# Performance work log

Hardware: AMD Instinct MI355X
Metric: run time of the kernel (lower is better)

The kernel has to match this reference:

```python
import jax, jax.numpy as jnp
import numpy as np

LORA_ALPHA = 2.0

def setup_inputs() -> dict:
    key = jax.random.key(0)
    k1, k2, k3, k4 = jax.random.split(key, 4)
    B, S, D_IN, D_OUT, R = 4, 2048, 4096, 4096, 16
    x = jax.random.normal(k1, (B, S, D_IN), dtype=jnp.float32)
    weight = jax.random.normal(k2, (D_OUT, D_IN), dtype=jnp.float32) * (1.0 / np.sqrt(D_IN))
    lora_A = jax.random.normal(k3, (R, D_IN), dtype=jnp.float32) * (1.0 / np.sqrt(D_IN))
    lora_B = jax.random.normal(k4, (D_OUT, R), dtype=jnp.float32) * 0.02
    return {"x": x, "weight": weight, "lora_A": lora_A, "lora_B": lora_B}

def reference(x, weight, lora_A, lora_B):
    # main_out = F.linear(x, weight) = x @ weight.T
    main_out = jnp.einsum('bsd,od->bso', x, weight)
    # Faithful to source: materialize lora_weight = B @ A (out x in), then full linear
    lora_weight = lora_B @ lora_A  # [out, in]
    lora_out = jnp.einsum('bsd,od->bso', x, lora_weight) * LORA_ALPHA
    return main_out + lora_out
```

## Files before the change

### kernel.cpp

```cpp
#include <hip/hip_runtime.h>
#include <stdint.h>

typedef __attribute__((ext_vector_type(8))) short bf16x8;
typedef __attribute__((ext_vector_type(4))) float f32x4;

#define GM 8192
#define GN 4096
#define GK 4096
#define KT32 (GK / 32)

__device__ __forceinline__ unsigned short f2bf(float f) {
  union { float f; unsigned int u; } c; c.f = f;
  unsigned int u = c.u;
  unsigned int r = u + 0x7FFFu + ((u >> 16) & 1u);
  return (unsigned short)(r >> 16);
}

__global__ __launch_bounds__(256) void cvt_x_kernel(const float* __restrict__ x,
                                                    unsigned short* __restrict__ xb) {
  int i = blockIdx.x * 256 + threadIdx.x;
  const float4* p = (const float4*)x + (size_t)i * 2;
  float4 a = p[0], b = p[1];
  unsigned short t[8] = { f2bf(a.x), f2bf(a.y), f2bf(a.z), f2bf(a.w),
                          f2bf(b.x), f2bf(b.y), f2bf(b.z), f2bf(b.w) };
  int4 pk; __builtin_memcpy(&pk, t, 16);
  ((int4*)xb)[i] = pk;
}

__global__ __launch_bounds__(256) void weff_kernel(const float* __restrict__ w,
                                                   const float* __restrict__ lA,
                                                   const float* __restrict__ lB,
                                                   unsigned short* __restrict__ wb) {
  const int K = GK;
  int idx = blockIdx.x * 256 + threadIdx.x;
  int cg = idx & 511;
  int rg = idx >> 9;
  int i0 = cg << 3;
  int o0 = rg << 3;

  float acc[8][8];
#pragma unroll
  for (int r = 0; r < 8; ++r)
#pragma unroll
    for (int c = 0; c < 8; ++c) acc[r][c] = 0.f;

#pragma unroll
  for (int r = 0; r < 16; ++r) {
    float4 a0 = *(const float4*)(lA + (size_t)r * K + i0);
    float4 a1 = *(const float4*)(lA + (size_t)r * K + i0 + 4);
    float av[8] = { a0.x, a0.y, a0.z, a0.w, a1.x, a1.y, a1.z, a1.w };
#pragma unroll
    for (int row = 0; row < 8; ++row) {
      float b = lB[(size_t)(o0 + row) * 16 + r];
#pragma unroll
      for (int c = 0; c < 8; ++c) acc[row][c] += b * av[c];
    }
  }

#pragma unroll
  for (int row = 0; row < 8; ++row) {
    float4 w0 = *(const float4*)(w + (size_t)(o0 + row) * K + i0);
    float4 w1 = *(const float4*)(w + (size_t)(o0 + row) * K + i0 + 4);
    unsigned short t[8] = {
      f2bf(w0.x + 2.0f * acc[row][0]), f2bf(w0.y + 2.0f * acc[row][1]),
      f2bf(w0.z + 2.0f * acc[row][2]), f2bf(w0.w + 2.0f * acc[row][3]),
      f2bf(w1.x + 2.0f * acc[row][4]), f2bf(w1.y + 2.0f * acc[row][5]),
      f2bf(w1.z + 2.0f * acc[row][6]), f2bf(w1.w + 2.0f * acc[row][7]) };
    int4 pk; __builtin_memcpy(&pk, t, 16);
    *(int4*)(wb + (size_t)(o0 + row) * K + i0) = pk;
  }
}


__device__ __forceinline__ void gload16(const unsigned short* g, char* l) {
  __builtin_amdgcn_global_load_lds((__attribute__((address_space(1))) void*)g,
                                   (__attribute__((address_space(3))) void*)l, 16, 0, 0);
}

__device__ __forceinline__ void bar() {
  asm volatile("" ::: "memory");
  __builtin_amdgcn_s_barrier();
  asm volatile("" ::: "memory");
}

template <int N>
__device__ __forceinline__ void vmwait() {
  if constexpr (N == 0)      asm volatile("s_waitcnt vmcnt(0)" ::: "memory");
  else if constexpr (N == 4) asm volatile("s_waitcnt vmcnt(4)" ::: "memory");
}

#define MFMA_BF16(a, b, c) __builtin_amdgcn_mfma_f32_16x16x32_bf16((a), (b), (c), 0, 0, 0)

template <int BUF>
__device__ __forceinline__ void stage_tile(const unsigned short* A, const unsigned short* B,
                                           char* smem, int bm0, int bn0, int w, int lane,
                                           int kt) {
  const int gcol = ((lane & 3) * 8) ^ ((lane & 32) ? 16 : 0);
  const int r = lane >> 2;
#pragma unroll
  for (int i = 0; i < 2; ++i) {
    const int sr = 2 * w + i;
    gload16(A + (size_t)(bm0 + sr * 16 + r) * GK + kt * 32 + gcol,
            smem + BUF * 32768 + (sr << 10));
    gload16(B + (size_t)(bn0 + sr * 16 + r) * GK + kt * 32 + gcol,
            smem + BUF * 32768 + 16384 + (sr << 10));
  }
}

__device__ __forceinline__ bf16x8 ldsA(const char* smem, int buf, int sr, int foff) {
  return *(const bf16x8*)(smem + buf * 32768 + (sr << 10) + foff);
}
__device__ __forceinline__ bf16x8 ldsB(const char* smem, int buf, int sr, int foff) {
  return *(const bf16x8*)(smem + buf * 32768 + 16384 + (sr << 10) + foff);
}

template <int BUF, int TAIL>
__device__ __forceinline__ void phase(const unsigned short* __restrict__ A,
                                      const unsigned short* __restrict__ B,
                                      char* smem, int bm0, int bn0, int w, int lane,
                                      int wm, int wn, int foff, int kt,
                                      f32x4 (&acc)[8][4]) {
  if constexpr (TAIL == 0)
    stage_tile<(BUF + 2) & 3>(A, B, smem, bm0, bn0, w, lane, kt + 2);

  bf16x8 av[8], bv[4];
#pragma unroll
  for (int mi = 0; mi < 8; ++mi) av[mi] = ldsA(smem, BUF, wm * 8 + mi, foff);
#pragma unroll
  for (int ni = 0; ni < 4; ++ni) bv[ni] = ldsB(smem, BUF, wn * 4 + ni, foff);

  if constexpr (TAIL == 0)      vmwait<4>();
  else if constexpr (TAIL == 1) vmwait<0>();
  bar();

  __builtin_amdgcn_s_setprio(1);
#pragma unroll
  for (int mi = 0; mi < 8; ++mi)
#pragma unroll
    for (int ni = 0; ni < 4; ++ni)
      acc[mi][ni] = MFMA_BF16(av[mi], bv[ni], acc[mi][ni]);
  __builtin_amdgcn_s_setprio(0);
}

__global__ __launch_bounds__(512, 2) void gemm_bt_kernel(const unsigned short* __restrict__ A,
                                                         const unsigned short* __restrict__ B,
                                                         float* __restrict__ C) {
  __shared__ alignas(16) char smem[131072];

  const int t = threadIdx.x, lane = t & 63, w = t >> 6;
  const int wm = w >> 2, wn = w & 3;

  const int bid = blockIdx.x;
  const int wg  = (bid & 7) * (512 / 8) + (bid >> 3);
  const int bx = wg & 15, by = wg >> 4;
  const int bm0 = by * 256, bn0 = bx * 256;

  int foff = (lane & 15) * 64 + ((lane >> 4) << 4);
  foff ^= ((foff >> 9) & 1) << 5;

  stage_tile<0>(A, B, smem, bm0, bn0, w, lane, 0);
  stage_tile<1>(A, B, smem, bm0, bn0, w, lane, 1);
  vmwait<4>();
  bar();

  f32x4 acc[8][4] = {};

  for (int kt = 0; kt < KT32 - 4; kt += 4) {
    phase<0, 0>(A, B, smem, bm0, bn0, w, lane, wm, wn, foff, kt,     acc);
    phase<1, 0>(A, B, smem, bm0, bn0, w, lane, wm, wn, foff, kt + 1, acc);
    phase<2, 0>(A, B, smem, bm0, bn0, w, lane, wm, wn, foff, kt + 2, acc);
    phase<3, 0>(A, B, smem, bm0, bn0, w, lane, wm, wn, foff, kt + 3, acc);
  }
  phase<0, 0>(A, B, smem, bm0, bn0, w, lane, wm, wn, foff, KT32 - 4, acc);
  phase<1, 0>(A, B, smem, bm0, bn0, w, lane, wm, wn, foff, KT32 - 3, acc);
  phase<2, 1>(A, B, smem, bm0, bn0, w, lane, wm, wn, foff, KT32 - 2, acc);
  phase<3, 2>(A, B, smem, bm0, bn0, w, lane, wm, wn, foff, KT32 - 1, acc);

  const int orow = (lane >> 4) << 2;
#pragma unroll
  for (int mi = 0; mi < 8; ++mi) {
#pragma unroll
    for (int ni = 0; ni < 4; ++ni) {
      float* cp = C + (size_t)(bm0 + wm * 128 + mi * 16 + orow) * GN
                    + (bn0 + wn * 64 + ni * 16 + (lane & 15));
#pragma unroll
      for (int r = 0; r < 4; ++r)
        cp[(size_t)r * GN] = acc[mi][ni][r];
    }
  }
}

extern "C" void kernel_launch(void* const* d_in, const int* in_sizes, int n_in,
                              void* d_out, int out_size, void* d_ws, size_t ws_size,
                              hipStream_t stream) {
  const float* x  = (const float*)d_in[0];
  const float* w  = (const float*)d_in[1];
  const float* lA = (const float*)d_in[2];
  const float* lB = (const float*)d_in[3];
  float* out = (float*)d_out;

  const int M = GM, N = GN, K = GK;

  unsigned short* xb = (unsigned short*)d_ws;
  unsigned short* wb = xb + (size_t)M * K;

  cvt_x_kernel<<<dim3((M * K / 8) / 256), dim3(256), 0, stream>>>(x, xb);
  weff_kernel<<<dim3((N / 8) * (K / 8) / 256), dim3(256), 0, stream>>>(w, lA, lB, wb);
  gemm_bt_kernel<<<dim3((M / 256) * (N / 256)), dim3(512), 0, stream>>>(xb, wb, out);
}
```

Before: 293.6 us.

## Shrink GEMM block tile to 256x128 with triple-buffered LDS pipeline

Halves the block's N tile to 128 and the per-wave tile to 64x64. It switches from four to three LDS stage buffers, cutting shared memory from 128KB to 72KB so more blocks can be resident per CU. Loop unrolling and wait counts are adjusted for the 3-stage ring, and an explicit lgkmcnt wait is added before the barrier. This trades lower per-block data reuse (more global/L2 traffic per FLOP) for higher occupancy and latency hiding.

Result: slower. 340.3 us (+15.9%).

```diff
diff --git a/kernel.cpp b/kernel.cpp
--- a/kernel.cpp
+++ b/kernel.cpp
@@ -86,7 +86,11 @@
 template <int N>
 __device__ __forceinline__ void vmwait() {
   if constexpr (N == 0)      asm volatile("s_waitcnt vmcnt(0)" ::: "memory");
-  else if constexpr (N == 4) asm volatile("s_waitcnt vmcnt(4)" ::: "memory");
+  else if constexpr (N == 3) asm volatile("s_waitcnt vmcnt(3)" ::: "memory");
+}
+
+__device__ __forceinline__ void lgkm0() {
+  asm volatile("s_waitcnt lgkmcnt(0)" ::: "memory");
 }
 
 #define MFMA_BF16(a, b, c) __builtin_amdgcn_mfma_f32_16x16x32_bf16((a), (b), (c), 0, 0, 0)
@@ -97,91 +101,87 @@
                                            int kt) {
   const int gcol = ((lane & 3) * 8) ^ ((lane & 32) ? 16 : 0);
   const int r = lane >> 2;
-#pragma unroll
-  for (int i = 0; i < 2; ++i) {
-    const int sr = 2 * w + i;
-    gload16(A + (size_t)(bm0 + sr * 16 + r) * GK + kt * 32 + gcol,
-            smem + BUF * 32768 + (sr << 10));
-    gload16(B + (size_t)(bn0 + sr * 16 + r) * GK + kt * 32 + gcol,
-            smem + BUF * 32768 + 16384 + (sr << 10));
-  }
+  char* base = smem + BUF * 24576;
+  gload16(A + (size_t)(bm0 + (2 * w) * 16 + r) * GK + kt * 32 + gcol, base + ((2 * w) << 10));
+  gload16(A + (size_t)(bm0 + (2 * w + 1) * 16 + r) * GK + kt * 32 + gcol, base + ((2 * w + 1) << 10));
+  gload16(B + (size_t)(bn0 + w * 16 + r) * GK + kt * 32 + gcol, base + 16384 + (w << 10));
 }
 
 __device__ __forceinline__ bf16x8 ldsA(const char* smem, int buf, int sr, int foff) {
-  return *(const bf16x8*)(smem + buf * 32768 + (sr << 10) + foff);
+  return *(const bf16x8*)(smem + buf * 24576 + (sr << 10) + foff);
 }
 __device__ __forceinline__ bf16x8 ldsB(const char* smem, int buf, int sr, int foff) {
-  return *(const bf16x8*)(smem + buf * 32768 + 16384 + (sr << 10) + foff);
-}
-
-template <int BUF, int TAIL>
+  return *(const bf16x8*)(smem + buf * 24576 + 16384 + (sr << 10) + foff);
+}
+
+template <int BUF>
 __device__ __forceinline__ void phase(const unsigned short* __restrict__ A,
                                       const unsigned short* __restrict__ B,
                                       char* smem, int bm0, int bn0, int w, int lane,
                                       int wm, int wn, int foff, int kt,
-                                      f32x4 (&acc)[8][4]) {
-  if constexpr (TAIL == 0)
-    stage_tile<(BUF + 2) & 3>(A, B, smem, bm0, bn0, w, lane, kt + 2);
-
-  bf16x8 av[8], bv[4];
-#pragma unroll
-  for (int mi = 0; mi < 8; ++mi) av[mi] = ldsA(smem, BUF, wm * 8 + mi, foff);
+                                      f32x4 (&acc)[4][4]) {
+  if (kt + 2 < KT32)
+    stage_tile<(BUF + 2) % 3>(A, B, smem, bm0, bn0, w, lane, kt + 2);
+
+  bf16x8 av[4], bv[4];
+#pragma unroll
+  for (int mi = 0; mi < 4; ++mi) av[mi] = ldsA(smem, BUF, wm * 4 + mi, foff);
 #pragma unroll
   for (int ni = 0; ni < 4; ++ni) bv[ni] = ldsB(smem, BUF, wn * 4 + ni, foff);
 
-  if constexpr (TAIL == 0)      vmwait<4>();
-  else if constexpr (TAIL == 1) vmwait<0>();
+  if (kt + 2 < KT32)      vmwait<3>();
+  else if (kt + 1 < KT32) vmwait<0>();
+  lgkm0();
   bar();
 
   __builtin_amdgcn_s_setprio(1);
 #pragma unroll
-  for (int mi = 0; mi < 8; ++mi)
+  for (int mi = 0; mi < 4; ++mi)
 #pragma unroll
     for (int ni = 0; ni < 4; ++ni)
       acc[mi][ni] = MFMA_BF16(av[mi], bv[ni], acc[mi][ni]);
   __builtin_amdgcn_s_setprio(0);
 }
 
-__global__ __launch_bounds__(512, 2) void gemm_bt_kernel(const unsigned short* __restrict__ A,
+__global__ __launch_bounds__(512, 4) void gemm_bt_kernel(const unsigned short* __restrict__ A,
                                                          const unsigned short* __restrict__ B,
                                                          float* __restrict__ C) {
-  __shared__ alignas(16) char smem[131072];
+  __shared__ alignas(16) char smem[73728];
 
   const int t = threadIdx.x, lane = t & 63, w = t >> 6;
-  const int wm = w >> 2, wn = w & 3;
+  const int wm = w >> 1, wn = w & 1;
 
   const int bid = blockIdx.x;
-  const int wg  = (bid & 7) * (512 / 8) + (bid >> 3);
-  const int bx = wg & 15, by = wg >> 4;
-  const int bm0 = by * 256, bn0 = bx * 256;
+  const int wg  = (bid & 7) * (1024 / 8) + (bid >> 3);
+  const int bx = wg & 31, by = wg >> 5;
+  const int bm0 = by * 256, bn0 = bx * 128;
 
   int foff = (lane & 15) * 64 + ((lane >> 4) << 4);
   foff ^= ((foff >> 9) & 1) << 5;
 
   stage_tile<0>(A, B, smem, bm0, bn0, w, lane, 0);
   stage_tile<1>(A, B, smem, bm0, bn0, w, lane, 1);
-  vmwait<4>();
+  vmwait<3>();
   bar();
 
-  f32x4 acc[8][4] = {};
-
-  for (int kt = 0; kt < KT32 - 4; kt += 4) {
-    phase<0, 0>(A, B, smem, bm0, bn0, w, lane, wm, wn, foff, kt,     acc);
-    phase<1, 0>(A, B, smem, bm0, bn0, w, lane, wm, wn, foff, kt + 1, acc);
-    phase<2, 0>(A, B, smem, bm0, bn0, w, lane, wm, wn, foff, kt + 2, acc);
-    phase<3, 0>(A, B, smem, bm0, bn0, w, lane, wm, wn, foff, kt + 3, acc);
-  }
-  phase<0, 0>(A, B, smem, bm0, bn0, w, lane, wm, wn, foff, KT32 - 4, acc);
-  phase<1, 0>(A, B, smem, bm0, bn0, w, lane, wm, wn, foff, KT32 - 3, acc);
-  phase<2, 1>(A, B, smem, bm0, bn0, w, lane, wm, wn, foff, KT32 - 2, acc);
-  phase<3, 2>(A, B, smem, bm0, bn0, w, lane, wm, wn, foff, KT32 - 1, acc);
+  f32x4 acc[4][4] = {};
+
+  int kt = 0;
+  while (kt + 3 <= KT32) {
+    phase<0>(A, B, smem, bm0, bn0, w, lane, wm, wn, foff, kt,     acc);
+    phase<1>(A, B, smem, bm0, bn0, w, lane, wm, wn, foff, kt + 1, acc);
+    phase<2>(A, B, smem, bm0, bn0, w, lane, wm, wn, foff, kt + 2, acc);
+    kt += 3;
+  }
+  phase<0>(A, B, smem, bm0, bn0, w, lane, wm, wn, foff, 126, acc);
+  phase<1>(A, B, smem, bm0, bn0, w, lane, wm, wn, foff, 127, acc);
 
   const int orow = (lane >> 4) << 2;
 #pragma unroll
-  for (int mi = 0; mi < 8; ++mi) {
+  for (int mi = 0; mi < 4; ++mi) {
 #pragma unroll
     for (int ni = 0; ni < 4; ++ni) {
-      float* cp = C + (size_t)(bm0 + wm * 128 + mi * 16 + orow) * GN
+      float* cp = C + (size_t)(bm0 + wm * 64 + mi * 16 + orow) * GN
                     + (bn0 + wn * 64 + ni * 16 + (lane & 15));
 #pragma unroll
       for (int r = 0; r < 4; ++r)
@@ -206,5 +206,5 @@
 
   cvt_x_kernel<<<dim3((M * K / 8) / 256), dim3(256), 0, stream>>>(x, xb);
   weff_kernel<<<dim3((N / 8) * (K / 8) / 256), dim3(256), 0, stream>>>(w, lA, lB, wb);
-  gemm_bt_kernel<<<dim3((M / 256) * (N / 256)), dim3(512), 0, stream>>>(xb, wb, out);
-}
+  gemm_bt_kernel<<<dim3((M / 256) * (N / 128)), dim3(512), 0, stream>>>(xb, wb, out);
+}
```

## Switch GEMM to 32x32x16 MFMA with 64-wide K tiles and split staging

Applied to the files above, without the earlier changes.

Replaces the 16x16x32 bf16 MFMA tiling with 32x32x16 MFMA fragments, halving fragment loads per flop. K tiles grow to 64 with double-buffered 64KB stages, and each tile is staged in four interleaved quarter-loads spread across the compute phases. The aim is higher MFMA throughput per LDS read and smoother overlap of global-to-LDS loads with compute. The cost is more complex synchronisation, with one barrier per phase, and a changed epilogue write pattern.

New measurement: 321.6 us. +9.5%, slower.

```diff
diff --git a/kernel.cpp b/kernel.cpp
--- a/kernel.cpp
+++ b/kernel.cpp
@@ -2,12 +2,12 @@
 #include <stdint.h>
 
 typedef __attribute__((ext_vector_type(8))) short bf16x8;
-typedef __attribute__((ext_vector_type(4))) float f32x4;
+typedef __attribute__((ext_vector_type(16))) float f32x16;
 
 #define GM 8192
 #define GN 4096
 #define GK 4096
-#define KT32 (GK / 32)
+#define KTILES (GK / 64)
 
 __device__ __forceinline__ unsigned short f2bf(float f) {
   union { float f; unsigned int u; } c; c.f = f;
@@ -86,60 +86,92 @@
 template <int N>
 __device__ __forceinline__ void vmwait() {
   if constexpr (N == 0)      asm volatile("s_waitcnt vmcnt(0)" ::: "memory");
-  else if constexpr (N == 4) asm volatile("s_waitcnt vmcnt(4)" ::: "memory");
-}
-
-#define MFMA_BF16(a, b, c) __builtin_amdgcn_mfma_f32_16x16x32_bf16((a), (b), (c), 0, 0, 0)
-
-template <int BUF>
-__device__ __forceinline__ void stage_tile(const unsigned short* A, const unsigned short* B,
+  else if constexpr (N == 2) asm volatile("s_waitcnt vmcnt(2)" ::: "memory");
+}
+
+#define MFMA32(a, b, c) __builtin_amdgcn_mfma_f32_32x32x16_bf16((a), (b), (c), 0, 0, 0)
+
+template <int ISB, int SC, int BUF>
+__device__ __forceinline__ void stage_half(const unsigned short* A, const unsigned short* B,
                                            char* smem, int bm0, int bn0, int w, int lane,
                                            int kt) {
+  const unsigned short* mat = ISB ? B : A;
+  const int mbase = ISB ? bn0 : bm0;
   const int gcol = ((lane & 3) * 8) ^ ((lane & 32) ? 16 : 0);
-  const int r = lane >> 2;
 #pragma unroll
   for (int i = 0; i < 2; ++i) {
     const int sr = 2 * w + i;
-    gload16(A + (size_t)(bm0 + sr * 16 + r) * GK + kt * 32 + gcol,
-            smem + BUF * 32768 + (sr << 10));
-    gload16(B + (size_t)(bn0 + sr * 16 + r) * GK + kt * 32 + gcol,
-            smem + BUF * 32768 + 16384 + (sr << 10));
-  }
-}
-
-__device__ __forceinline__ bf16x8 ldsA(const char* smem, int buf, int sr, int foff) {
-  return *(const bf16x8*)(smem + buf * 32768 + (sr << 10) + foff);
-}
-__device__ __forceinline__ bf16x8 ldsB(const char* smem, int buf, int sr, int foff) {
-  return *(const bf16x8*)(smem + buf * 32768 + 16384 + (sr << 10) + foff);
-}
-
-template <int BUF, int TAIL>
-__device__ __forceinline__ void phase(const unsigned short* __restrict__ A,
+    const unsigned short* src = mat + (size_t)(mbase + sr * 16 + (lane >> 2)) * GK
+                                    + kt * 64 + SC * 32 + gcol;
+    char* dst = smem + BUF * 65536 + ISB * 32768 + ((sr * 2 + SC) << 10);
+    gload16(src, dst);
+  }
+}
+
+__device__ __forceinline__ bf16x8 ldsFrag(const char* smem, int byteOff) {
+  return *(const bf16x8*)(smem + byteOff);
+}
+
+template <int CUR, int TAIL>
+__device__ __forceinline__ void ktile(const unsigned short* __restrict__ A,
                                       const unsigned short* __restrict__ B,
                                       char* smem, int bm0, int bn0, int w, int lane,
-                                      int wm, int wn, int foff, int kt,
-                                      f32x4 (&acc)[8][4]) {
-  if constexpr (TAIL == 0)
-    stage_tile<(BUF + 2) & 3>(A, B, smem, bm0, bn0, w, lane, kt + 2);
-
-  bf16x8 av[8], bv[4];
-#pragma unroll
-  for (int mi = 0; mi < 8; ++mi) av[mi] = ldsA(smem, BUF, wm * 8 + mi, foff);
-#pragma unroll
-  for (int ni = 0; ni < 4; ++ni) bv[ni] = ldsB(smem, BUF, wn * 4 + ni, foff);
-
-  if constexpr (TAIL == 0)      vmwait<4>();
+                                      int wm, int wn, int kt,
+                                      f32x16 (&acc)[4][2]) {
+  constexpr int NXT = CUR ^ 1;
+  const int rlo = lane & 15, sub2 = (lane >> 4) & 1, khalf = lane >> 5;
+  const int m32 = (rlo & 8) << 2;
+
+  bf16x8 av[4], bv[2];
+
+#define READ_PHASE(PH, BUF)                                                            \
+  {                                                                                    \
+    constexpr int SC = (PH) >> 1;                                                      \
+    const int kin = ((PH) & 1) * 32 + khalf * 16;                                      \
+    const int roff = (rlo * 64 + kin) ^ m32;                                           \
+    _Pragma("unroll")                                                                  \
+    for (int mi = 0; mi < 4; ++mi)                                                     \
+      av[mi] = ldsFrag(smem, (BUF) * 65536 +                                           \
+                       (((wm * 8 + mi * 2 + sub2) * 2 + SC) << 10) + roff);            \
+    _Pragma("unroll")                                                                  \
+    for (int ni = 0; ni < 2; ++ni)                                                     \
+      bv[ni] = ldsFrag(smem, (BUF) * 65536 + 32768 +                                   \
+                       (((wn * 4 + ni * 2 + sub2) * 2 + SC) << 10) + roff);            \
+  }
+
+#define MFMA_PHASE()                                                                   \
+  __builtin_amdgcn_s_setprio(1);                                                       \
+  _Pragma("unroll")                                                                    \
+  for (int mi = 0; mi < 4; ++mi) {                                                     \
+    acc[mi][0] = MFMA32(av[mi], bv[0], acc[mi][0]);                                    \
+    acc[mi][1] = MFMA32(av[mi], bv[1], acc[mi][1]);                                    \
+  }                                                                                    \
+  __builtin_amdgcn_s_setprio(0);
+
+  if constexpr (TAIL < 2) stage_half<1, 0, NXT>(A, B, smem, bm0, bn0, w, lane, kt + 1);
+  READ_PHASE(0, CUR);
+  bar();
+  MFMA_PHASE();
+
+  if constexpr (TAIL < 2) stage_half<0, 1, NXT>(A, B, smem, bm0, bn0, w, lane, kt + 1);
+  READ_PHASE(1, CUR);
+  bar();
+  MFMA_PHASE();
+
+  if constexpr (TAIL < 2) stage_half<1, 1, NXT>(A, B, smem, bm0, bn0, w, lane, kt + 1);
+  READ_PHASE(2, CUR);
+  bar();
+  MFMA_PHASE();
+
+  if constexpr (TAIL == 0) stage_half<0, 0, CUR>(A, B, smem, bm0, bn0, w, lane, kt + 2);
+  READ_PHASE(3, CUR);
+  if constexpr (TAIL == 0)      vmwait<2>();
   else if constexpr (TAIL == 1) vmwait<0>();
   bar();
-
-  __builtin_amdgcn_s_setprio(1);
-#pragma unroll
-  for (int mi = 0; mi < 8; ++mi)
-#pragma unroll
-    for (int ni = 0; ni < 4; ++ni)
-      acc[mi][ni] = MFMA_BF16(av[mi], bv[ni], acc[mi][ni]);
-  __builtin_amdgcn_s_setprio(0);
+  MFMA_PHASE();
+
+#undef READ_PHASE
+#undef MFMA_PHASE
 }
 
 __global__ __launch_bounds__(512, 2) void gemm_bt_kernel(const unsigned short* __restrict__ A,
@@ -155,37 +187,36 @@
   const int bx = wg & 15, by = wg >> 4;
   const int bm0 = by * 256, bn0 = bx * 256;
 
-  int foff = (lane & 15) * 64 + ((lane >> 4) << 4);
-  foff ^= ((foff >> 9) & 1) << 5;
-
-  stage_tile<0>(A, B, smem, bm0, bn0, w, lane, 0);
-  stage_tile<1>(A, B, smem, bm0, bn0, w, lane, 1);
-  vmwait<4>();
-  bar();
-
-  f32x4 acc[8][4] = {};
-
-  for (int kt = 0; kt < KT32 - 4; kt += 4) {
-    phase<0, 0>(A, B, smem, bm0, bn0, w, lane, wm, wn, foff, kt,     acc);
-    phase<1, 0>(A, B, smem, bm0, bn0, w, lane, wm, wn, foff, kt + 1, acc);
-    phase<2, 0>(A, B, smem, bm0, bn0, w, lane, wm, wn, foff, kt + 2, acc);
-    phase<3, 0>(A, B, smem, bm0, bn0, w, lane, wm, wn, foff, kt + 3, acc);
-  }
-  phase<0, 0>(A, B, smem, bm0, bn0, w, lane, wm, wn, foff, KT32 - 4, acc);
-  phase<1, 0>(A, B, smem, bm0, bn0, w, lane, wm, wn, foff, KT32 - 3, acc);
-  phase<2, 1>(A, B, smem, bm0, bn0, w, lane, wm, wn, foff, KT32 - 2, acc);
-  phase<3, 2>(A, B, smem, bm0, bn0, w, lane, wm, wn, foff, KT32 - 1, acc);
-
-  const int orow = (lane >> 4) << 2;
-#pragma unroll
-  for (int mi = 0; mi < 8; ++mi) {
-#pragma unroll
-    for (int ni = 0; ni < 4; ++ni) {
-      float* cp = C + (size_t)(bm0 + wm * 128 + mi * 16 + orow) * GN
-                    + (bn0 + wn * 64 + ni * 16 + (lane & 15));
-#pragma unroll
-      for (int r = 0; r < 4; ++r)
-        cp[(size_t)r * GN] = acc[mi][ni][r];
+  stage_half<0, 0, 0>(A, B, smem, bm0, bn0, w, lane, 0);
+  stage_half<1, 0, 0>(A, B, smem, bm0, bn0, w, lane, 0);
+  stage_half<0, 1, 0>(A, B, smem, bm0, bn0, w, lane, 0);
+  stage_half<1, 1, 0>(A, B, smem, bm0, bn0, w, lane, 0);
+  stage_half<0, 0, 1>(A, B, smem, bm0, bn0, w, lane, 1);
+  vmwait<2>();
+  bar();
+
+  f32x16 acc[4][2] = {};
+
+  for (int kt = 0; kt < KTILES - 2; kt += 2) {
+    ktile<0, 0>(A, B, smem, bm0, bn0, w, lane, wm, wn, kt,     acc);
+    ktile<1, 0>(A, B, smem, bm0, bn0, w, lane, wm, wn, kt + 1, acc);
+  }
+  ktile<0, 1>(A, B, smem, bm0, bn0, w, lane, wm, wn, KTILES - 2, acc);
+  ktile<1, 2>(A, B, smem, bm0, bn0, w, lane, wm, wn, KTILES - 1, acc);
+
+  const int ocol = lane & 31;
+  const int radd = (lane >> 5) << 2;
+#pragma unroll
+  for (int mi = 0; mi < 4; ++mi) {
+#pragma unroll
+    for (int ni = 0; ni < 2; ++ni) {
+      float* cp = C + (size_t)(bm0 + wm * 128 + mi * 32 + radd) * GN
+                    + (bn0 + wn * 64 + ni * 32 + ocol);
+#pragma unroll
+      for (int r = 0; r < 16; ++r) {
+        const int row = (r & 3) + 8 * (r >> 2);
+        cp[(size_t)row * GN] = acc[mi][ni][r];
+      }
     }
   }
 }
```
